# Kernel tuning notes

Hardware: AMD Instinct MI355X
Metric: run time of the kernel (lower is better)

## Reference

```python
import jax, jax.numpy as jnp
import numpy as np

HIDDEN = 1024
QUERY = 1024
NUM_EXPERTS = 64
TOP_K = 2

def setup_inputs() -> dict:
    key = jax.random.key(0)
    k1, k2, k3 = jax.random.split(key, 3)
    B, total, num_tokens = 8, 128, 576
    vis_emb = jax.random.normal(k1, (total, num_tokens, HIDDEN), dtype=jnp.float32)
    query_emb = jax.random.normal(k2, (B, QUERY), dtype=jnp.float32)
    # nn.Linear default init scale ~ 1/sqrt(fan_in)
    W_gate = jax.random.normal(k3, (NUM_EXPERTS, HIDDEN + QUERY), dtype=jnp.float32) / np.sqrt(HIDDEN + QUERY)
    return {"vis_emb": vis_emb, "query_emb": query_emb, "W_gate": W_gate}

def reference(vis_emb, query_emb, W_gate):
    # Faithful to: cat([vis, query_expanded], -1) @ W.T, but expressed as two
    # split matmuls (identical math, avoids materializing the concat).
    total = vis_emb.shape[0]
    B = query_emb.shape[0]
    repeat = total // B
    W_vis = W_gate[:, :HIDDEN]    # [E, H]
    W_qry = W_gate[:, HIDDEN:]    # [E, Q]
    vis_logits = jnp.einsum('nth,eh->nte', vis_emb, W_vis)          # [total, T, E]
    qry_logits = jnp.einsum('bq,eq->be', query_emb, W_qry)          # [B, E]
    qry_logits = jnp.repeat(qry_logits, repeat, axis=0)[:, None, :]  # [total, 1, E]
    gate_logits = vis_logits + qry_logits                            # [total, T, E]
    gate_scores = jax.nn.softmax(gate_logits, axis=-1)
    topk_scores, topk_idx = jax.lax.top_k(gate_scores, TOP_K)
    return (topk_scores, topk_idx, gate_scores, gate_logits)
```

## Files before the change

### kernel.cpp

```cpp
#include <hip/hip_runtime.h>
#include <math.h>

#define HIDDEN 1024

typedef _Float16 half8 __attribute__((ext_vector_type(8)));
typedef float floatx4 __attribute__((ext_vector_type(4)));

#define OUT_TKS 0
#define OUT_TKI 147456
#define OUT_GS  294912
#define OUT_GL  5013504

#define QL_FOFF 65536

__global__ __launch_bounds__(256) void prep_kernel(
    const float* __restrict__ query_emb, const float* __restrict__ W_gate,
    float* __restrict__ ws) {
  const int bid = blockIdx.x, tid = threadIdx.x;
  if (bid < 64) {
    _Float16* WH = (_Float16*)ws;
    _Float16* WL = WH + 65536;
    const int base = (bid * 256 + tid) * 4;
    #pragma unroll
    for (int u = 0; u < 4; ++u) {
      const int idx = base + u;
      const int j  = idx & 7;
      const int L  = (idx >> 3) & 63;
      const int nt = (idx >> 9) & 3;
      const int c  = idx >> 11;
      const int e  = nt * 16 + (L & 15);
      const int k  = c * 32 + (L >> 4) * 8 + j;
      const float w = W_gate[e * 2048 + k];
      const _Float16 hi = (_Float16)w;
      const float hif = (float)hi;
      WH[idx] = hi;
      WL[idx] = (_Float16)((w - hif) * 2048.0f);
    }
  } else {
    const int b = bid - 64;
    const int e = tid >> 2, qq = tid & 3;
    const float* qp = query_emb + b * 1024 + qq * 256;
    const float* wp = W_gate + e * 2048 + 1024 + qq * 256;
    float s = 0.f;
    #pragma unroll 4
    for (int j = 0; j < 256; j += 4) {
      const float4 a = *(const float4*)(qp + j);
      const float4 w = *(const float4*)(wp + j);
      s += a.x * w.x + a.y * w.y + a.z * w.z + a.w * w.w;
    }
    s += __shfl_xor(s, 1);
    s += __shfl_xor(s, 2);
    if (qq == 0) ws[QL_FOFF + b * 64 + e] = s;
  }
}

__global__ __launch_bounds__(256, 3) void router_main(
    const float* __restrict__ vis, const float* __restrict__ ws,
    float* __restrict__ out) {
  const int tid = threadIdx.x;
  const int L  = tid & 63;
  const int wv = tid >> 6;
  const int m  = L & 15;
  const int q  = L >> 4;
  const long t0 = (long)blockIdx.x * 64 + wv * 16;
  const _Float16* WH = (const _Float16*)ws;
  const _Float16* WL = WH + 65536;
  const float* QL = ws + QL_FOFF;

  const float* ap = vis + (t0 + m) * HIDDEN + q * 8;
  const int fo = L * 8;

  floatx4 acc[4], accx[4];
  #pragma unroll
  for (int nt = 0; nt < 4; ++nt) {
    acc[nt]  = (floatx4){0.f, 0.f, 0.f, 0.f};
    accx[nt] = (floatx4){0.f, 0.f, 0.f, 0.f};
  }

  float4 a0 = *(const float4*)ap;
  float4 a1 = *(const float4*)(ap + 4);

  for (int c = 0; c < 32; ++c) {
    const float* apn = ap + ((c < 31) ? 32 : 0);
    const float4 n0 = *(const float4*)apn;
    const float4 n1 = *(const float4*)(apn + 4);

    half8 ah, al;
    {
      const float av[8] = {a0.x, a0.y, a0.z, a0.w, a1.x, a1.y, a1.z, a1.w};
      #pragma unroll
      for (int j = 0; j < 8; ++j) {
        const _Float16 h = (_Float16)av[j];
        ah[j] = h;
        al[j] = (_Float16)((av[j] - (float)h) * 2048.0f);
      }
    }

    const _Float16* whp = WH + (c * 4) * 512 + fo;
    const _Float16* wlp = WL + (c * 4) * 512 + fo;
    #pragma unroll
    for (int nt = 0; nt < 4; ++nt) {
      const half8 wh = *(const half8*)(whp + nt * 512);
      const half8 wl = *(const half8*)(wlp + nt * 512);
      acc[nt]  = __builtin_amdgcn_mfma_f32_16x16x32_f16(ah, wh, acc[nt],  0, 0, 0);
      accx[nt] = __builtin_amdgcn_mfma_f32_16x16x32_f16(ah, wl, accx[nt], 0, 0, 0);
      accx[nt] = __builtin_amdgcn_mfma_f32_16x16x32_f16(al, wh, accx[nt], 0, 0, 0);
    }

    ap = apn;
    a0 = n0; a1 = n1;
  }

  const int bq = blockIdx.x / 144;
  float ql[4];
  #pragma unroll
  for (int nt = 0; nt < 4; ++nt) ql[nt] = QL[bq * 64 + nt * 16 + m];

  float* out_tks = out + OUT_TKS;
  float* out_tki = out + OUT_TKI;
  float* out_gs  = out + OUT_GS;
  float* out_gl  = out + OUT_GL;

  #pragma unroll
  for (int i = 0; i < 4; ++i) {
    const long tok = t0 + q * 4 + i;
    float l[4];
    #pragma unroll
    for (int nt = 0; nt < 4; ++nt)
      l[nt] = acc[nt][i] + accx[nt][i] * (1.0f / 2048.0f) + ql[nt];
    #pragma unroll
    for (int nt = 0; nt < 4; ++nt)
      out_gl[tok * 64 + nt * 16 + m] = l[nt];

    float mx = fmaxf(fmaxf(l[0], l[1]), fmaxf(l[2], l[3]));
    mx = fmaxf(mx, __shfl_xor(mx, 1));
    mx = fmaxf(mx, __shfl_xor(mx, 2));
    mx = fmaxf(mx, __shfl_xor(mx, 4));
    mx = fmaxf(mx, __shfl_xor(mx, 8));

    float s[4], ssum = 0.f;
    #pragma unroll
    for (int nt = 0; nt < 4; ++nt) { s[nt] = expf(l[nt] - mx); ssum += s[nt]; }
    ssum += __shfl_xor(ssum, 1);
    ssum += __shfl_xor(ssum, 2);
    ssum += __shfl_xor(ssum, 4);
    ssum += __shfl_xor(ssum, 8);
    const float inv = 1.0f / ssum;
    #pragma unroll
    for (int nt = 0; nt < 4; ++nt) s[nt] *= inv;
    #pragma unroll
    for (int nt = 0; nt < 4; ++nt)
      out_gs[tok * 64 + nt * 16 + m] = s[nt];

    float v1 = s[0], v2 = s[1]; int i1 = m, i2 = 16 + m;
    if (s[1] > v1) { v2 = v1; i2 = i1; v1 = s[1]; i1 = 16 + m; }
    if (s[2] > v1)      { v2 = v1; i2 = i1; v1 = s[2]; i1 = 32 + m; }
    else if (s[2] > v2) { v2 = s[2]; i2 = 32 + m; }
    if (s[3] > v1)      { v2 = v1; i2 = i1; v1 = s[3]; i1 = 48 + m; }
    else if (s[3] > v2) { v2 = s[3]; i2 = 48 + m; }

    #pragma unroll
    for (int msk = 1; msk < 16; msk <<= 1) {
      const float w1 = __shfl_xor(v1, msk), w2 = __shfl_xor(v2, msk);
      const int   j1 = __shfl_xor(i1, msk), j2 = __shfl_xor(i2, msk);
      const bool wfirst = (w1 > v1) || (w1 == v1 && j1 < i1);
      if (wfirst) {
        const bool vsec = (v1 > w2) || (v1 == w2 && i1 < j2);
        v2 = vsec ? v1 : w2; i2 = vsec ? i1 : j2;
        v1 = w1; i1 = j1;
      } else {
        const bool wsec = (w1 > v2) || (w1 == v2 && j1 < i2);
        if (wsec) { v2 = w1; i2 = j1; }
      }
    }
    if (m == 0) {
      *(float2*)(out_tks + tok * 2) = make_float2(v1, v2);
      *(float2*)(out_tki + tok * 2) = make_float2((float)i1, (float)i2);
    }
  }
}

extern "C" void kernel_launch(void* const* d_in, const int* in_sizes, int n_in,
                              void* d_out, int out_size, void* d_ws, size_t ws_size,
                              hipStream_t stream) {
  const float* vis   = (const float*)d_in[0];
  const float* query = (const float*)d_in[1];
  const float* wg    = (const float*)d_in[2];
  float* ws = (float*)d_ws;
  float* o  = (float*)d_out;
  hipLaunchKernelGGL(prep_kernel, dim3(72), dim3(256), 0, stream, query, wg, ws);
  hipLaunchKernelGGL(router_main, dim3(1152), dim3(256), 0, stream, vis, ws, o);
}
```

Measured before the change: 494.9 us.

## Deepen software prefetch of activations and weights, shrink blocks to two waves

The main loop now prefetches activation rows two K-chunks ahead and the fp16 hi/lo weight fragments one chunk ahead in registers, so the MFMAs no longer wait on same-iteration global loads. Blocks shrink from 256 to 128 threads (32 tokens each), the grid doubles to 2304, and the per-batch index divisor is updated to match. The occupancy hint in launch bounds is dropped, so register use can grow with the extra prefetch buffers, which may lower the number of waves per CU.

```diff
diff --git a/kernel.cpp b/kernel.cpp
--- a/kernel.cpp
+++ b/kernel.cpp
@@ -54,7 +54,7 @@
   }
 }
 
-__global__ __launch_bounds__(256, 3) void router_main(
+__global__ __launch_bounds__(128) void router_main(
     const float* __restrict__ vis, const float* __restrict__ ws,
     float* __restrict__ out) {
   const int tid = threadIdx.x;
@@ -62,12 +62,12 @@
   const int wv = tid >> 6;
   const int m  = L & 15;
   const int q  = L >> 4;
-  const long t0 = (long)blockIdx.x * 64 + wv * 16;
+  const long t0 = (long)blockIdx.x * 32 + wv * 16;
   const _Float16* WH = (const _Float16*)ws;
   const _Float16* WL = WH + 65536;
   const float* QL = ws + QL_FOFF;
 
-  const float* ap = vis + (t0 + m) * HIDDEN + q * 8;
+  const float* abase = vis + (t0 + m) * HIDDEN + q * 8;
   const int fo = L * 8;
 
   floatx4 acc[4], accx[4];
@@ -77,17 +77,41 @@
     accx[nt] = (floatx4){0.f, 0.f, 0.f, 0.f};
   }
 
-  float4 a0 = *(const float4*)ap;
-  float4 a1 = *(const float4*)(ap + 4);
-
+  float4 a0c = *(const float4*)(abase);
+  float4 a1c = *(const float4*)(abase + 4);
+  float4 a0n = *(const float4*)(abase + 32);
+  float4 a1n = *(const float4*)(abase + 36);
+  half8 bh0 = *(const half8*)(WH + fo);
+  half8 bh1 = *(const half8*)(WH + fo + 512);
+  half8 bh2 = *(const half8*)(WH + fo + 1024);
+  half8 bh3 = *(const half8*)(WH + fo + 1536);
+  half8 bl0 = *(const half8*)(WL + fo);
+  half8 bl1 = *(const half8*)(WL + fo + 512);
+  half8 bl2 = *(const half8*)(WL + fo + 1024);
+  half8 bl3 = *(const half8*)(WL + fo + 1536);
+
+  #pragma unroll 2
   for (int c = 0; c < 32; ++c) {
-    const float* apn = ap + ((c < 31) ? 32 : 0);
-    const float4 n0 = *(const float4*)apn;
-    const float4 n1 = *(const float4*)(apn + 4);
+    const int c2 = (c < 30) ? (c + 2) : c;
+    const float* ap2 = abase + c2 * 32;
+    const float4 f0 = *(const float4*)ap2;
+    const float4 f1 = *(const float4*)(ap2 + 4);
+
+    const int c1 = (c < 31) ? (c + 1) : c;
+    const _Float16* whp = WH + c1 * 2048 + fo;
+    const _Float16* wlp = WL + c1 * 2048 + fo;
+    const half8 nh0 = *(const half8*)(whp);
+    const half8 nh1 = *(const half8*)(whp + 512);
+    const half8 nh2 = *(const half8*)(whp + 1024);
+    const half8 nh3 = *(const half8*)(whp + 1536);
+    const half8 nl0 = *(const half8*)(wlp);
+    const half8 nl1 = *(const half8*)(wlp + 512);
+    const half8 nl2 = *(const half8*)(wlp + 1024);
+    const half8 nl3 = *(const half8*)(wlp + 1536);
 
     half8 ah, al;
     {
-      const float av[8] = {a0.x, a0.y, a0.z, a0.w, a1.x, a1.y, a1.z, a1.w};
+      const float av[8] = {a0c.x, a0c.y, a0c.z, a0c.w, a1c.x, a1c.y, a1c.z, a1c.w};
       #pragma unroll
       for (int j = 0; j < 8; ++j) {
         const _Float16 h = (_Float16)av[j];
@@ -96,22 +120,25 @@
       }
     }
 
-    const _Float16* whp = WH + (c * 4) * 512 + fo;
-    const _Float16* wlp = WL + (c * 4) * 512 + fo;
-    #pragma unroll
-    for (int nt = 0; nt < 4; ++nt) {
-      const half8 wh = *(const half8*)(whp + nt * 512);
-      const half8 wl = *(const half8*)(wlp + nt * 512);
-      acc[nt]  = __builtin_amdgcn_mfma_f32_16x16x32_f16(ah, wh, acc[nt],  0, 0, 0);
-      accx[nt] = __builtin_amdgcn_mfma_f32_16x16x32_f16(ah, wl, accx[nt], 0, 0, 0);
-      accx[nt] = __builtin_amdgcn_mfma_f32_16x16x32_f16(al, wh, accx[nt], 0, 0, 0);
-    }
-
-    ap = apn;
-    a0 = n0; a1 = n1;
-  }
-
-  const int bq = blockIdx.x / 144;
+    acc[0]  = __builtin_amdgcn_mfma_f32_16x16x32_f16(ah, bh0, acc[0],  0, 0, 0);
+    accx[0] = __builtin_amdgcn_mfma_f32_16x16x32_f16(ah, bl0, accx[0], 0, 0, 0);
+    accx[0] = __builtin_amdgcn_mfma_f32_16x16x32_f16(al, bh0, accx[0], 0, 0, 0);
+    acc[1]  = __builtin_amdgcn_mfma_f32_16x16x32_f16(ah, bh1, acc[1],  0, 0, 0);
+    accx[1] = __builtin_amdgcn_mfma_f32_16x16x32_f16(ah, bl1, accx[1], 0, 0, 0);
+    accx[1] = __builtin_amdgcn_mfma_f32_16x16x32_f16(al, bh1, accx[1], 0, 0, 0);
+    acc[2]  = __builtin_amdgcn_mfma_f32_16x16x32_f16(ah, bh2, acc[2],  0, 0, 0);
+    accx[2] = __builtin_amdgcn_mfma_f32_16x16x32_f16(ah, bl2, accx[2], 0, 0, 0);
+    accx[2] = __builtin_amdgcn_mfma_f32_16x16x32_f16(al, bh2, accx[2], 0, 0, 0);
+    acc[3]  = __builtin_amdgcn_mfma_f32_16x16x32_f16(ah, bh3, acc[3],  0, 0, 0);
+    accx[3] = __builtin_amdgcn_mfma_f32_16x16x32_f16(ah, bl3, accx[3], 0, 0, 0);
+    accx[3] = __builtin_amdgcn_mfma_f32_16x16x32_f16(al, bh3, accx[3], 0, 0, 0);
+
+    a0c = a0n; a1c = a1n; a0n = f0; a1n = f1;
+    bh0 = nh0; bh1 = nh1; bh2 = nh2; bh3 = nh3;
+    bl0 = nl0; bl1 = nl1; bl2 = nl2; bl3 = nl3;
+  }
+
+  const int bq = blockIdx.x / 288;
   float ql[4];
   #pragma unroll
   for (int nt = 0; nt < 4; ++nt) ql[nt] = QL[bq * 64 + nt * 16 + m];
@@ -189,5 +216,5 @@
   float* ws = (float*)d_ws;
   float* o  = (float*)d_out;
   hipLaunchKernelGGL(prep_kernel, dim3(72), dim3(256), 0, stream, query, wg, ws);
-  hipLaunchKernelGGL(router_main, dim3(1152), dim3(256), 0, stream, vis, ws, o);
+  hipLaunchKernelGGL(router_main, dim3(2304), dim3(128), 0, stream, vis, ws, o);
 }
```

Result: faster. 466.8 us (-5.7%).

## Give each wave two M-fragments to reuse weight loads; add nontemporal loads/stores

Applied to the files above, without the earlier changes.

Each 64-thread block now computes 32 tokens as two 16-row MFMA fragments that share the same loaded weight fragments. This halves weight traffic per token and doubles MFMA work per load. Activation loads and the logit/score stores become nontemporal to avoid polluting cache with streamed data. The grid changes to 2304 single-wave blocks, and the higher accumulator count raises register pressure and may lower occupancy.

```diff
diff --git a/kernel.cpp b/kernel.cpp
--- a/kernel.cpp
+++ b/kernel.cpp
@@ -5,6 +5,7 @@
 
 typedef _Float16 half8 __attribute__((ext_vector_type(8)));
 typedef float floatx4 __attribute__((ext_vector_type(4)));
+typedef float floatv4 __attribute__((ext_vector_type(4)));
 
 #define OUT_TKS 0
 #define OUT_TKI 147456
@@ -54,64 +55,81 @@
   }
 }
 
-__global__ __launch_bounds__(256, 3) void router_main(
+static __device__ __forceinline__ floatv4 ntld4(const float* p) {
+  return __builtin_nontemporal_load((const floatv4*)p);
+}
+
+__global__ __launch_bounds__(64, 3) void router_main(
     const float* __restrict__ vis, const float* __restrict__ ws,
     float* __restrict__ out) {
-  const int tid = threadIdx.x;
-  const int L  = tid & 63;
-  const int wv = tid >> 6;
+  const int L  = threadIdx.x & 63;
   const int m  = L & 15;
   const int q  = L >> 4;
-  const long t0 = (long)blockIdx.x * 64 + wv * 16;
+  const long t0 = (long)blockIdx.x * 32;
   const _Float16* WH = (const _Float16*)ws;
   const _Float16* WL = WH + 65536;
   const float* QL = ws + QL_FOFF;
 
-  const float* ap = vis + (t0 + m) * HIDDEN + q * 8;
+  const float* ab0 = vis + (t0 + m) * HIDDEN + q * 8;
+  const float* ab1 = ab0 + 16 * HIDDEN;
   const int fo = L * 8;
 
-  floatx4 acc[4], accx[4];
+  floatx4 acc[2][4], accx[2][4];
   #pragma unroll
-  for (int nt = 0; nt < 4; ++nt) {
-    acc[nt]  = (floatx4){0.f, 0.f, 0.f, 0.f};
-    accx[nt] = (floatx4){0.f, 0.f, 0.f, 0.f};
+  for (int mf = 0; mf < 2; ++mf)
+    #pragma unroll
+    for (int nt = 0; nt < 4; ++nt) {
+      acc[mf][nt]  = (floatx4){0.f, 0.f, 0.f, 0.f};
+      accx[mf][nt] = (floatx4){0.f, 0.f, 0.f, 0.f};
+    }
+
+  floatv4 c00 = ntld4(ab0), c01 = ntld4(ab0 + 4);
+  floatv4 c10 = ntld4(ab1), c11 = ntld4(ab1 + 4);
+
+  #pragma unroll 2
+  for (int c = 0; c < 32; ++c) {
+    const _Float16* whp = WH + c * 2048 + fo;
+    const _Float16* wlp = WL + c * 2048 + fo;
+    half8 bh[4], bl[4];
+    #pragma unroll
+    for (int nt = 0; nt < 4; ++nt) {
+      bh[nt] = *(const half8*)(whp + nt * 512);
+      bl[nt] = *(const half8*)(wlp + nt * 512);
+    }
+
+    const int cn = (c < 31) ? (c + 1) : c;
+    const floatv4 n00 = ntld4(ab0 + cn * 32), n01 = ntld4(ab0 + cn * 32 + 4);
+    const floatv4 n10 = ntld4(ab1 + cn * 32), n11 = ntld4(ab1 + cn * 32 + 4);
+
+    half8 ah0, al0, ah1, al1;
+    {
+      const float a0v[8] = {c00.x, c00.y, c00.z, c00.w, c01.x, c01.y, c01.z, c01.w};
+      const float a1v[8] = {c10.x, c10.y, c10.z, c10.w, c11.x, c11.y, c11.z, c11.w};
+      #pragma unroll
+      for (int j = 0; j < 8; ++j) {
+        const _Float16 h0 = (_Float16)a0v[j];
+        ah0[j] = h0;
+        al0[j] = (_Float16)((a0v[j] - (float)h0) * 2048.0f);
+        const _Float16 h1 = (_Float16)a1v[j];
+        ah1[j] = h1;
+        al1[j] = (_Float16)((a1v[j] - (float)h1) * 2048.0f);
+      }
+    }
+
+    #pragma unroll
+    for (int nt = 0; nt < 4; ++nt) {
+      acc[0][nt]  = __builtin_amdgcn_mfma_f32_16x16x32_f16(ah0, bh[nt], acc[0][nt],  0, 0, 0);
+      acc[1][nt]  = __builtin_amdgcn_mfma_f32_16x16x32_f16(ah1, bh[nt], acc[1][nt],  0, 0, 0);
+      accx[0][nt] = __builtin_amdgcn_mfma_f32_16x16x32_f16(ah0, bl[nt], accx[0][nt], 0, 0, 0);
+      accx[1][nt] = __builtin_amdgcn_mfma_f32_16x16x32_f16(ah1, bl[nt], accx[1][nt], 0, 0, 0);
+      accx[0][nt] = __builtin_amdgcn_mfma_f32_16x16x32_f16(al0, bh[nt], accx[0][nt], 0, 0, 0);
+      accx[1][nt] = __builtin_amdgcn_mfma_f32_16x16x32_f16(al1, bh[nt], accx[1][nt], 0, 0, 0);
+    }
+
+    c00 = n00; c01 = n01; c10 = n10; c11 = n11;
   }
 
-  float4 a0 = *(const float4*)ap;
-  float4 a1 = *(const float4*)(ap + 4);
-
-  for (int c = 0; c < 32; ++c) {
-    const float* apn = ap + ((c < 31) ? 32 : 0);
-    const float4 n0 = *(const float4*)apn;
-    const float4 n1 = *(const float4*)(apn + 4);
-
-    half8 ah, al;
-    {
-      const float av[8] = {a0.x, a0.y, a0.z, a0.w, a1.x, a1.y, a1.z, a1.w};
-      #pragma unroll
-      for (int j = 0; j < 8; ++j) {
-        const _Float16 h = (_Float16)av[j];
-        ah[j] = h;
-        al[j] = (_Float16)((av[j] - (float)h) * 2048.0f);
-      }
-    }
-
-    const _Float16* whp = WH + (c * 4) * 512 + fo;
-    const _Float16* wlp = WL + (c * 4) * 512 + fo;
-    #pragma unroll
-    for (int nt = 0; nt < 4; ++nt) {
-      const half8 wh = *(const half8*)(whp + nt * 512);
-      const half8 wl = *(const half8*)(wlp + nt * 512);
-      acc[nt]  = __builtin_amdgcn_mfma_f32_16x16x32_f16(ah, wh, acc[nt],  0, 0, 0);
-      accx[nt] = __builtin_amdgcn_mfma_f32_16x16x32_f16(ah, wl, accx[nt], 0, 0, 0);
-      accx[nt] = __builtin_amdgcn_mfma_f32_16x16x32_f16(al, wh, accx[nt], 0, 0, 0);
-    }
-
-    ap = apn;
-    a0 = n0; a1 = n1;
-  }
-
-  const int bq = blockIdx.x / 144;
+  const int bq = blockIdx.x / 288;
   float ql[4];
   #pragma unroll
   for (int nt = 0; nt < 4; ++nt) ql[nt] = QL[bq * 64 + nt * 16 + m];
@@ -122,60 +140,63 @@
   float* out_gl  = out + OUT_GL;
 
   #pragma unroll
-  for (int i = 0; i < 4; ++i) {
-    const long tok = t0 + q * 4 + i;
-    float l[4];
-    #pragma unroll
-    for (int nt = 0; nt < 4; ++nt)
-      l[nt] = acc[nt][i] + accx[nt][i] * (1.0f / 2048.0f) + ql[nt];
-    #pragma unroll
-    for (int nt = 0; nt < 4; ++nt)
-      out_gl[tok * 64 + nt * 16 + m] = l[nt];
-
-    float mx = fmaxf(fmaxf(l[0], l[1]), fmaxf(l[2], l[3]));
-    mx = fmaxf(mx, __shfl_xor(mx, 1));
-    mx = fmaxf(mx, __shfl_xor(mx, 2));
-    mx = fmaxf(mx, __shfl_xor(mx, 4));
-    mx = fmaxf(mx, __shfl_xor(mx, 8));
-
-    float s[4], ssum = 0.f;
-    #pragma unroll
-    for (int nt = 0; nt < 4; ++nt) { s[nt] = expf(l[nt] - mx); ssum += s[nt]; }
-    ssum += __shfl_xor(ssum, 1);
-    ssum += __shfl_xor(ssum, 2);
-    ssum += __shfl_xor(ssum, 4);
-    ssum += __shfl_xor(ssum, 8);
-    const float inv = 1.0f / ssum;
-    #pragma unroll
-    for (int nt = 0; nt < 4; ++nt) s[nt] *= inv;
-    #pragma unroll
-    for (int nt = 0; nt < 4; ++nt)
-      out_gs[tok * 64 + nt * 16 + m] = s[nt];
-
-    float v1 = s[0], v2 = s[1]; int i1 = m, i2 = 16 + m;
-    if (s[1] > v1) { v2 = v1; i2 = i1; v1 = s[1]; i1 = 16 + m; }
-    if (s[2] > v1)      { v2 = v1; i2 = i1; v1 = s[2]; i1 = 32 + m; }
-    else if (s[2] > v2) { v2 = s[2]; i2 = 32 + m; }
-    if (s[3] > v1)      { v2 = v1; i2 = i1; v1 = s[3]; i1 = 48 + m; }
-    else if (s[3] > v2) { v2 = s[3]; i2 = 48 + m; }
-
-    #pragma unroll
-    for (int msk = 1; msk < 16; msk <<= 1) {
-      const float w1 = __shfl_xor(v1, msk), w2 = __shfl_xor(v2, msk);
-      const int   j1 = __shfl_xor(i1, msk), j2 = __shfl_xor(i2, msk);
-      const bool wfirst = (w1 > v1) || (w1 == v1 && j1 < i1);
-      if (wfirst) {
-        const bool vsec = (v1 > w2) || (v1 == w2 && i1 < j2);
-        v2 = vsec ? v1 : w2; i2 = vsec ? i1 : j2;
-        v1 = w1; i1 = j1;
-      } else {
-        const bool wsec = (w1 > v2) || (w1 == v2 && j1 < i2);
-        if (wsec) { v2 = w1; i2 = j1; }
+  for (int mf = 0; mf < 2; ++mf) {
+    #pragma unroll
+    for (int i = 0; i < 4; ++i) {
+      const long tok = t0 + mf * 16 + q * 4 + i;
+      float l[4];
+      #pragma unroll
+      for (int nt = 0; nt < 4; ++nt)
+        l[nt] = acc[mf][nt][i] + accx[mf][nt][i] * (1.0f / 2048.0f) + ql[nt];
+      #pragma unroll
+      for (int nt = 0; nt < 4; ++nt)
+        __builtin_nontemporal_store(l[nt], out_gl + tok * 64 + nt * 16 + m);
+
+      float mx = fmaxf(fmaxf(l[0], l[1]), fmaxf(l[2], l[3]));
+      mx = fmaxf(mx, __shfl_xor(mx, 1));
+      mx = fmaxf(mx, __shfl_xor(mx, 2));
+      mx = fmaxf(mx, __shfl_xor(mx, 4));
+      mx = fmaxf(mx, __shfl_xor(mx, 8));
+
+      float s[4], ssum = 0.f;
+      #pragma unroll
+      for (int nt = 0; nt < 4; ++nt) { s[nt] = expf(l[nt] - mx); ssum += s[nt]; }
+      ssum += __shfl_xor(ssum, 1);
+      ssum += __shfl_xor(ssum, 2);
+      ssum += __shfl_xor(ssum, 4);
+      ssum += __shfl_xor(ssum, 8);
+      const float inv = 1.0f / ssum;
+      #pragma unroll
+      for (int nt = 0; nt < 4; ++nt) s[nt] *= inv;
+      #pragma unroll
+      for (int nt = 0; nt < 4; ++nt)
+        __builtin_nontemporal_store(s[nt], out_gs + tok * 64 + nt * 16 + m);
+
+      float v1 = s[0], v2 = s[1]; int i1 = m, i2 = 16 + m;
+      if (s[1] > v1) { v2 = v1; i2 = i1; v1 = s[1]; i1 = 16 + m; }
+      if (s[2] > v1)      { v2 = v1; i2 = i1; v1 = s[2]; i1 = 32 + m; }
+      else if (s[2] > v2) { v2 = s[2]; i2 = 32 + m; }
+      if (s[3] > v1)      { v2 = v1; i2 = i1; v1 = s[3]; i1 = 48 + m; }
+      else if (s[3] > v2) { v2 = s[3]; i2 = 48 + m; }
+
+      #pragma unroll
+      for (int msk = 1; msk < 16; msk <<= 1) {
+        const float w1 = __shfl_xor(v1, msk), w2 = __shfl_xor(v2, msk);
+        const int   j1 = __shfl_xor(i1, msk), j2 = __shfl_xor(i2, msk);
+        const bool wfirst = (w1 > v1) || (w1 == v1 && j1 < i1);
+        if (wfirst) {
+          const bool vsec = (v1 > w2) || (v1 == w2 && i1 < j2);
+          v2 = vsec ? v1 : w2; i2 = vsec ? i1 : j2;
+          v1 = w1; i1 = j1;
+        } else {
+          const bool wsec = (w1 > v2) || (w1 == v2 && j1 < i2);
+          if (wsec) { v2 = w1; i2 = j1; }
+        }
       }
-    }
-    if (m == 0) {
-      *(float2*)(out_tks + tok * 2) = make_float2(v1, v2);
-      *(float2*)(out_tki + tok * 2) = make_float2((float)i1, (float)i2);
+      if (m == 0) {
+        *(float2*)(out_tks + tok * 2) = make_float2(v1, v2);
+        *(float2*)(out_tki + tok * 2) = make_float2((float)i1, (float)i2);
+      }
     }
   }
 }
@@ -189,5 +210,5 @@
   float* ws = (float*)d_ws;
   float* o  = (float*)d_out;
   hipLaunchKernelGGL(prep_kernel, dim3(72), dim3(256), 0, stream, query, wg, ws);
-  hipLaunchKernelGGL(router_main, dim3(1152), dim3(256), 0, stream, vis, ws, o);
-}
+  hipLaunchKernelGGL(router_main, dim3(2304), dim3(64), 0, stream, vis, ws, o);
+}
```

New measurement: 453.0 us. -8.5%, faster.
